# Kernel tuning notes

Hardware: AMD Instinct MI355X
Metric: run time of the kernel (lower is better)

## Reference

```python
import jax, jax.numpy as jnp
import numpy as np

N_NODES = 100000


def _gcn_conv(x, src, dst, ew, W, b, n_nodes):
    # PyG GCNConv: x' = D^{-1/2} (A + I) D^{-1/2} (x W) + b, with edge weights.
    h = x @ W  # [N, out]
    deg = jax.ops.segment_sum(ew, dst, num_segments=n_nodes)  # weighted in-degree
    dinv = jnp.where(deg > 0, jax.lax.rsqrt(deg), 0.0)
    norm = dinv[src] * ew * dinv[dst]  # [E]
    msg = h[src] * norm[:, None]  # gather + scale
    out = jax.ops.segment_sum(msg, dst, num_segments=n_nodes)  # scatter-add
    return out + b


def setup_inputs() -> dict:
    key = jax.random.key(0)
    ks = jax.random.split(key, 10)
    E = 1600000
    D_IN, H1, H2, D_OUT = 512, 128, 64, 1
    x = jax.random.normal(ks[0], (N_NODES, D_IN), dtype=jnp.float32)
    edge_index = jax.random.randint(ks[1], (2, E), 0, N_NODES, dtype=jnp.int64)
    edge_attr = jax.random.uniform(ks[2], (E,), dtype=jnp.float32)
    def glorot(k, fan_in, fan_out):
        s = jnp.sqrt(6.0 / (fan_in + fan_out))
        return jax.random.uniform(k, (fan_in, fan_out), minval=-s, maxval=s, dtype=jnp.float32)
    return {
        "x": x,
        "edge_index": edge_index,
        "edge_attr": edge_attr,
        "W1": glorot(ks[3], D_IN, H1), "b1": jnp.zeros((H1,), jnp.float32),
        "W2": glorot(ks[4], H1, H2), "b2": jnp.zeros((H2,), jnp.float32),
        "W3": glorot(ks[5], H2, D_OUT), "b3": jnp.zeros((D_OUT,), jnp.float32),
    }


def reference(x, edge_index, edge_attr, W1, b1, W2, b2, W3, b3):
    n = x.shape[0]
    # add self-loops with weight 1 (PyG GCNConv default)
    loops = jnp.arange(n, dtype=edge_index.dtype)
    src = jnp.concatenate([edge_index[0], loops])
    dst = jnp.concatenate([edge_index[1], loops])
    ew = jnp.concatenate([edge_attr, jnp.ones((n,), edge_attr.dtype)])
    h = _gcn_conv(x, src, dst, ew, W1, b1, n)
    h = jax.nn.relu(h)  # dropout is identity in eval mode
    h = _gcn_conv(h, src, dst, ew, W2, b2, n)
    h = jax.nn.relu(h)
    out = _gcn_conv(h, src, dst, ew, W3, b3, n)
    return out
```

## Files before the change

kernel.cpp:

```cpp
#include <hip/hip_runtime.h>

typedef __attribute__((ext_vector_type(4))) float f32x4;
typedef __attribute__((ext_vector_type(8))) short bf16x8;
typedef __attribute__((ext_vector_type(4))) unsigned short u16x4;

__device__ __forceinline__ unsigned short f2bf(float f) {
  unsigned int u = __builtin_bit_cast(unsigned int, f);
  u += 0x7fffu + ((u >> 16) & 1u);
  return (unsigned short)(u >> 16);
}
__device__ __forceinline__ float bf2f(unsigned short h) {
  unsigned int u = ((unsigned int)h) << 16;
  return __builtin_bit_cast(float, u);
}
__device__ __forceinline__ float bflo(unsigned int u) { return bf2f((unsigned short)(u & 0xffffu)); }
__device__ __forceinline__ float bfhi(unsigned int u) { return bf2f((unsigned short)(u >> 16)); }
__device__ __forceinline__ unsigned int packbf(float a, float b) {
  return (unsigned int)f2bf(a) | ((unsigned int)f2bf(b) << 16);
}

__global__ void hist_rank_k(const int* __restrict__ dst, int* __restrict__ cnt,
                            int* __restrict__ rank, int E) {
  int e = blockIdx.x * blockDim.x + threadIdx.x;
  if (e < E) rank[e] = atomicAdd(&cnt[dst[e]], 1);
}

__global__ void scan1_k(const int* __restrict__ cnt, int* __restrict__ row,
                        int* __restrict__ bsum, int N) {
  __shared__ int sh[256];
  const int tid = threadIdx.x;
  const int base = blockIdx.x * 2048 + tid * 8;
  int v[8]; int s = 0;
#pragma unroll
  for (int i = 0; i < 8; ++i) {
    int idx = base + i;
    v[i] = (idx < N) ? cnt[idx] : 0;
    s += v[i];
  }
  sh[tid] = s;
  __syncthreads();
  for (int off = 1; off < 256; off <<= 1) {
    int t = (tid >= off) ? sh[tid - off] : 0;
    __syncthreads();
    sh[tid] += t;
    __syncthreads();
  }
  int excl = sh[tid] - s;
  if (tid == 255) bsum[blockIdx.x] = sh[255];
  int run = excl;
#pragma unroll
  for (int i = 0; i < 8; ++i) {
    int idx = base + i;
    if (idx < N) row[idx] = run;
    run += v[i];
  }
}
__global__ void scan2_k(int* __restrict__ bsum, int nb) {
  if (threadIdx.x == 0 && blockIdx.x == 0) {
    int run = 0;
    for (int i = 0; i < nb; ++i) { int t = bsum[i]; bsum[i] = run; run += t; }
  }
}
__global__ void scan3_k(int* __restrict__ row, const int* __restrict__ bsum, int N, int E) {
  int idx = blockIdx.x * blockDim.x + threadIdx.x;
  if (idx < N) row[idx] += bsum[idx >> 11];
  if (idx == N) row[N] = E;
}
__global__ void scatter_nr_k(const int* __restrict__ src, const int* __restrict__ dst,
                             const float* __restrict__ ew, const int* __restrict__ row,
                             const int* __restrict__ rank, uint2* __restrict__ eadj, int E) {
  int e = blockIdx.x * blockDim.x + threadIdx.x;
  if (e >= E) return;
  int pos = row[dst[e]] + rank[e];
  eadj[pos] = make_uint2((unsigned)src[e], __builtin_bit_cast(unsigned, ew[e]));
}
__global__ void deg_dinv_k(const int* __restrict__ row, const uint2* __restrict__ eadj,
                           float* __restrict__ dinv, int N) {
  int n = blockIdx.x * blockDim.x + threadIdx.x;
  if (n >= N) return;
  float s = 1.0f;
  int end = row[n + 1];
  for (int e = row[n]; e < end; ++e) s += __builtin_bit_cast(float, eadj[e].y);
  dinv[n] = rsqrtf(s);
}
__global__ void fixnorm_k(const int* __restrict__ row, uint2* __restrict__ eadj,
                          const float* __restrict__ dinv, int N) {
  int n = blockIdx.x * blockDim.x + threadIdx.x;
  if (n >= N) return;
  float dd = dinv[n];
  int end = row[n + 1];
  for (int e = row[n]; e < end; ++e) {
    uint2 m = eadj[e];
    float nm = __builtin_bit_cast(float, m.y) * dinv[m.x] * dd;
    eadj[e].y = __builtin_bit_cast(unsigned, nm);
  }
}
__global__ void conv_wt2_k(const float* __restrict__ W1, unsigned short* __restrict__ Wt1,
                           const float* __restrict__ W2, unsigned short* __restrict__ Wt2) {
  int idx = blockIdx.x * blockDim.x + threadIdx.x;
  if (idx < 512 * 128) {
    int n = idx >> 9, k = idx & 511;
    Wt1[idx] = f2bf(W1[k * 128 + n]);
  } else {
    int j = idx - 512 * 128;
    if (j < 128 * 64) {
      int n = j >> 7, k = j & 127;
      Wt2[j] = f2bf(W2[k * 64 + n]);
    }
  }
}

template<int NC, int KD>
__launch_bounds__(256, 2)
__global__ void gemm_f32a_k(const float* __restrict__ A, const unsigned short* __restrict__ Wt,
                            unsigned short* __restrict__ Hb, int M) {
  constexpr int BM = 128, BK = 64;
  constexpr int WN = 64;
  constexpr int WGN = NC / WN;
  constexpr int WGM = 4 / WGN;
  constexpr int WM = BM / WGM;
  constexpr int FM = WM / 16;
  constexpr int FN = WN / 16;
  constexpr int KSUB = BK / 32;
  constexpr int A_PER_T = BM * (BK / 4) / 256;
  constexpr int B_PER_T = NC * (BK / 8) / 256;
  constexpr int nT = KD / BK;

  __shared__ unsigned short As[BM * BK];
  __shared__ unsigned short Bs[NC * BK];
  char* asb = reinterpret_cast<char*>(As);
  char* bsb = reinterpret_cast<char*>(Bs);

  const int tid = threadIdx.x;
  const int lane = tid & 63;
  const int wid = tid >> 6;
  const int wr = wid / WGN;
  const int wc = wid % WGN;
  const int lg = lane >> 4;
  const int lr = lane & 15;
  const int blockM = blockIdx.x * BM;

  float4 areg[A_PER_T];
  uint4 breg[B_PER_T];

  auto load_tiles = [&](int k0) {
#pragma unroll
    for (int i = 0; i < A_PER_T; ++i) {
      int chunk = tid + i * 256;
      int r = chunk >> 4, c4 = chunk & 15;
      int gr = blockM + r; if (gr >= M) gr = M - 1;
      areg[i] = *reinterpret_cast<const float4*>(A + (size_t)gr * KD + k0 + c4 * 4);
    }
#pragma unroll
    for (int i = 0; i < B_PER_T; ++i) {
      int chunk = tid + i * 256;
      int n = chunk >> 3, c = chunk & 7;
      breg[i] = *reinterpret_cast<const uint4*>(Wt + (size_t)n * KD + k0 + c * 8);
    }
  };

  f32x4 acc[FM][FN] = {};
  load_tiles(0);

  for (int t = 0; t < nT; ++t) {
    __syncthreads();
#pragma unroll
    for (int i = 0; i < A_PER_T; ++i) {
      int chunk = tid + i * 256;
      int r = chunk >> 4, c4 = chunk & 15;
      float4 v = areg[i];
      u16x4 p = { f2bf(v.x), f2bf(v.y), f2bf(v.z), f2bf(v.w) };
      int byte = r * (BK * 2) + ((c4 * 8) ^ ((r & 7) << 4));
      *reinterpret_cast<u16x4*>(asb + byte) = p;
    }
#pragma unroll
    for (int i = 0; i < B_PER_T; ++i) {
      int chunk = tid + i * 256;
      int n = chunk >> 3, c = chunk & 7;
      int byte = n * (BK * 2) + ((c * 16) ^ ((n & 7) << 4));
      *reinterpret_cast<uint4*>(bsb + byte) = breg[i];
    }
    __syncthreads();
    if (t + 1 < nT) load_tiles((t + 1) * BK);

    bf16x8 af[FM][KSUB], bfr[FN][KSUB];
#pragma unroll
    for (int fm = 0; fm < FM; ++fm)
#pragma unroll
      for (int kk = 0; kk < KSUB; ++kk) {
        int row = wr * WM + fm * 16 + lr;
        int k = kk * 32 + lg * 8;
        int byte = row * (BK * 2) + ((k * 2) ^ ((row & 7) << 4));
        af[fm][kk] = *reinterpret_cast<const bf16x8*>(asb + byte);
      }
#pragma unroll
    for (int fn = 0; fn < FN; ++fn)
#pragma unroll
      for (int kk = 0; kk < KSUB; ++kk) {
        int n = wc * WN + fn * 16 + lr;
        int k = kk * 32 + lg * 8;
        int byte = n * (BK * 2) + ((k * 2) ^ ((n & 7) << 4));
        bfr[fn][kk] = *reinterpret_cast<const bf16x8*>(bsb + byte);
      }
#pragma unroll
    for (int kk = 0; kk < KSUB; ++kk)
#pragma unroll
      for (int fm = 0; fm < FM; ++fm)
#pragma unroll
        for (int fn = 0; fn < FN; ++fn)
          acc[fm][fn] = __builtin_amdgcn_mfma_f32_16x16x32_bf16(
              af[fm][kk], bfr[fn][kk], acc[fm][fn], 0, 0, 0);
  }

#pragma unroll
  for (int fm = 0; fm < FM; ++fm)
#pragma unroll
    for (int fn = 0; fn < FN; ++fn) {
      int col = wc * WN + fn * 16 + lr;
#pragma unroll
      for (int j = 0; j < 4; ++j) {
        int row = blockM + wr * WM + fm * 16 + lg * 4 + j;
        if (row < M)
          Hb[(size_t)row * NC + col] = f2bf(acc[fm][fn][j]);
      }
    }
}

__launch_bounds__(256, 2)
__global__ void gemm_bf16a_k(const unsigned short* __restrict__ A,
                             const unsigned short* __restrict__ Wt,
                             unsigned short* __restrict__ Hb, int M) {
  constexpr int BM = 128, BK = 64, NC = 64, KD = 128;
  constexpr int WM = 32;
  constexpr int FM = 2, FN = 4, KSUB = 2;
  constexpr int A_PER_T = 4;
  constexpr int B_PER_T = 2;
  constexpr int nT = KD / BK;

  __shared__ unsigned short As[BM * BK];
  __shared__ unsigned short Bs[NC * BK];
  char* asb = reinterpret_cast<char*>(As);
  char* bsb = reinterpret_cast<char*>(Bs);

  const int tid = threadIdx.x;
  const int lane = tid & 63;
  const int wid = tid >> 6;
  const int lg = lane >> 4;
  const int lr = lane & 15;
  const int blockM = blockIdx.x * BM;

  uint4 areg[A_PER_T];
  uint4 breg[B_PER_T];

  auto load_tiles = [&](int k0) {
#pragma unroll
    for (int i = 0; i < A_PER_T; ++i) {
      int chunk = tid + i * 256;
      int r = chunk >> 3, c = chunk & 7;
      int gr = blockM + r; if (gr >= M) gr = M - 1;
      areg[i] = *reinterpret_cast<const uint4*>(A + (size_t)gr * KD + k0 + c * 8);
    }
#pragma unroll
    for (int i = 0; i < B_PER_T; ++i) {
      int chunk = tid + i * 256;
      int n = chunk >> 3, c = chunk & 7;
      breg[i] = *reinterpret_cast<const uint4*>(Wt + (size_t)n * KD + k0 + c * 8);
    }
  };

  f32x4 acc[FM][FN] = {};
  load_tiles(0);

  for (int t = 0; t < nT; ++t) {
    __syncthreads();
#pragma unroll
    for (int i = 0; i < A_PER_T; ++i) {
      int chunk = tid + i * 256;
      int r = chunk >> 3, c = chunk & 7;
      int byte = r * (BK * 2) + ((c * 16) ^ ((r & 7) << 4));
      *reinterpret_cast<uint4*>(asb + byte) = areg[i];
    }
#pragma unroll
    for (int i = 0; i < B_PER_T; ++i) {
      int chunk = tid + i * 256;
      int n = chunk >> 3, c = chunk & 7;
      int byte = n * (BK * 2) + ((c * 16) ^ ((n & 7) << 4));
      *reinterpret_cast<uint4*>(bsb + byte) = breg[i];
    }
    __syncthreads();
    if (t + 1 < nT) load_tiles((t + 1) * BK);

    bf16x8 af[FM][KSUB], bfr[FN][KSUB];
#pragma unroll
    for (int fm = 0; fm < FM; ++fm)
#pragma unroll
      for (int kk = 0; kk < KSUB; ++kk) {
        int row = wid * WM + fm * 16 + lr;
        int k = kk * 32 + lg * 8;
        int byte = row * (BK * 2) + ((k * 2) ^ ((row & 7) << 4));
        af[fm][kk] = *reinterpret_cast<const bf16x8*>(asb + byte);
      }
#pragma unroll
    for (int fn = 0; fn < FN; ++fn)
#pragma unroll
      for (int kk = 0; kk < KSUB; ++kk) {
        int n = fn * 16 + lr;
        int k = kk * 32 + lg * 8;
        int byte = n * (BK * 2) + ((k * 2) ^ ((n & 7) << 4));
        bfr[fn][kk] = *reinterpret_cast<const bf16x8*>(bsb + byte);
      }
#pragma unroll
    for (int kk = 0; kk < KSUB; ++kk)
#pragma unroll
      for (int fm = 0; fm < FM; ++fm)
#pragma unroll
        for (int fn = 0; fn < FN; ++fn)
          acc[fm][fn] = __builtin_amdgcn_mfma_f32_16x16x32_bf16(
              af[fm][kk], bfr[fn][kk], acc[fm][fn], 0, 0, 0);
  }

#pragma unroll
  for (int fm = 0; fm < FM; ++fm)
#pragma unroll
    for (int fn = 0; fn < FN; ++fn) {
      int col = fn * 16 + lr;
#pragma unroll
      for (int j = 0; j < 4; ++j) {
        int row = blockM + wid * WM + fm * 16 + lg * 4 + j;
        if (row < M)
          Hb[(size_t)row * NC + col] = f2bf(acc[fm][fn][j]);
      }
    }
}

__global__ void agg_csr128_k(const int* __restrict__ row, const uint2* __restrict__ eadj,
                             const unsigned short* __restrict__ h, const float* __restrict__ bias,
                             const float* __restrict__ dinv, unsigned int* __restrict__ o1b, int N) {
  const int lane = threadIdx.x & 63;
  const int node = blockIdx.x * (blockDim.x >> 6) + (threadIdx.x >> 6);
  if (node >= N) return;
  const unsigned int* hu = reinterpret_cast<const unsigned int*>(h);
  const int beg = row[node], end = row[node + 1];
  const float di = dinv[node];
  const float di2 = di * di;
  unsigned int hv = hu[(size_t)node * 64 + lane];
  float acc0 = bflo(hv) * di2;
  float acc1 = bfhi(hv) * di2;
  int e = beg;
  for (; e + 4 <= end; e += 4) {
    uint2 m0 = eadj[e], m1 = eadj[e + 1], m2 = eadj[e + 2], m3 = eadj[e + 3];
    int s0 = __builtin_amdgcn_readfirstlane(m0.x);
    int s1 = __builtin_amdgcn_readfirstlane(m1.x);
    int s2 = __builtin_amdgcn_readfirstlane(m2.x);
    int s3 = __builtin_amdgcn_readfirstlane(m3.x);
    float n0 = __builtin_bit_cast(float, __builtin_amdgcn_readfirstlane(m0.y));
    float n1 = __builtin_bit_cast(float, __builtin_amdgcn_readfirstlane(m1.y));
    float n2 = __builtin_bit_cast(float, __builtin_amdgcn_readfirstlane(m2.y));
    float n3 = __builtin_bit_cast(float, __builtin_amdgcn_readfirstlane(m3.y));
    unsigned int h0 = hu[(size_t)s0 * 64 + lane];
    unsigned int h1 = hu[(size_t)s1 * 64 + lane];
    unsigned int h2 = hu[(size_t)s2 * 64 + lane];
    unsigned int h3 = hu[(size_t)s3 * 64 + lane];
    acc0 += bflo(h0) * n0 + bflo(h1) * n1 + bflo(h2) * n2 + bflo(h3) * n3;
    acc1 += bfhi(h0) * n0 + bfhi(h1) * n1 + bfhi(h2) * n2 + bfhi(h3) * n3;
  }
  for (; e < end; ++e) {
    uint2 m0 = eadj[e];
    int s0 = __builtin_amdgcn_readfirstlane(m0.x);
    float n0 = __builtin_bit_cast(float, __builtin_amdgcn_readfirstlane(m0.y));
    unsigned int h0 = hu[(size_t)s0 * 64 + lane];
    acc0 += bflo(h0) * n0;
    acc1 += bfhi(h0) * n0;
  }
  float2 b = reinterpret_cast<const float2*>(bias)[lane];
  float r0 = fmaxf(acc0 + b.x, 0.f);
  float r1 = fmaxf(acc1 + b.y, 0.f);
  o1b[(size_t)node * 64 + lane] = packbf(r0, r1);
}

__global__ void agg_l23_k(const int* __restrict__ row, const uint2* __restrict__ eadj,
                          const unsigned short* __restrict__ h2, const float* __restrict__ b2,
                          const float* __restrict__ W3, const float* __restrict__ dinv,
                          float* __restrict__ h3, int N) {
  const int lane = threadIdx.x & 63;
  const int half = lane >> 5;
  const int l = lane & 31;
  const int node = blockIdx.x * (blockDim.x >> 6) + (threadIdx.x >> 6);
  if (node >= N) return;
  const unsigned int* hu = reinterpret_cast<const unsigned int*>(h2);
  const int beg = row[node], end = row[node + 1];
  float acc0 = 0.f, acc1 = 0.f;
  {
    const float di = dinv[node];
    unsigned int hv = hu[(size_t)node * 32 + l];
    float di2 = (half == 0) ? di * di : 0.f;
    acc0 = bflo(hv) * di2;
    acc1 = bfhi(hv) * di2;
  }
  int e = beg + half;
  for (; e + 2 < end; e += 4) {
    uint2 ma = eadj[e], mb = eadj[e + 2];
    float na = __builtin_bit_cast(float, ma.y);
    float nb = __builtin_bit_cast(float, mb.y);
    unsigned int ha = hu[(size_t)ma.x * 32 + l];
    unsigned int hb = hu[(size_t)mb.x * 32 + l];
    acc0 += bflo(ha) * na + bflo(hb) * nb;
    acc1 += bfhi(ha) * na + bfhi(hb) * nb;
  }
  if (e < end) {
    uint2 ma = eadj[e];
    float na = __builtin_bit_cast(float, ma.y);
    unsigned int ha = hu[(size_t)ma.x * 32 + l];
    acc0 += bflo(ha) * na;
    acc1 += bfhi(ha) * na;
  }
  acc0 += __shfl_xor(acc0, 32, 64);
  acc1 += __shfl_xor(acc1, 32, 64);
  float2 bb = reinterpret_cast<const float2*>(b2)[l];
  float2 w3 = reinterpret_cast<const float2*>(W3)[l];
  float v = fmaxf(acc0 + bb.x, 0.f) * w3.x + fmaxf(acc1 + bb.y, 0.f) * w3.y;
#pragma unroll
  for (int off = 16; off > 0; off >>= 1) v += __shfl_xor(v, off, 64);
  if (lane == 0) h3[node] = v;
}

__global__ void agg_csr1_k(const int* __restrict__ row, const uint2* __restrict__ eadj,
                           const float* __restrict__ h3, const float* __restrict__ b3,
                           const float* __restrict__ dinv, float* __restrict__ out, int N) {
  int n = blockIdx.x * blockDim.x + threadIdx.x;
  if (n >= N) return;
  float di = dinv[n];
  float acc = h3[n] * di * di;
  const int beg = row[n], end = row[n + 1];
  int e = beg;
  for (; e + 2 <= end; e += 2) {
    uint2 m0 = eadj[e], m1 = eadj[e + 1];
    acc += h3[m0.x] * __builtin_bit_cast(float, m0.y)
         + h3[m1.x] * __builtin_bit_cast(float, m1.y);
  }
  if (e < end) {
    uint2 m = eadj[e];
    acc += h3[m.x] * __builtin_bit_cast(float, m.y);
  }
  out[n] = acc + b3[0];
}

extern "C" void kernel_launch(void* const* d_in, const int* in_sizes, int n_in,
                              void* d_out, int out_size, void* d_ws, size_t ws_size,
                              hipStream_t stream) {
  const float* x  = (const float*)d_in[0];
  const int*   ei = (const int*)d_in[1];
  const float* ea = (const float*)d_in[2];
  const float* W1 = (const float*)d_in[3];
  const float* b1 = (const float*)d_in[4];
  const float* W2 = (const float*)d_in[5];
  const float* b2 = (const float*)d_in[6];
  const float* W3 = (const float*)d_in[7];
  const float* b3 = (const float*)d_in[8];
  float* out = (float*)d_out;

  const int N = in_sizes[0] / 512;
  const int E = in_sizes[2];
  const int* src = ei;
  const int* dst = ei + E;

  char* w = (char*)d_ws;
  auto alloc = [&](size_t bytes) {
    char* p = w; w += (bytes + 511) & ~(size_t)511; return p;
  };
  float* dinv         = (float*)alloc((size_t)N * 4);
  int*   cnt          = (int*)alloc((size_t)N * 4);
  int*   rowp         = (int*)alloc((size_t)(N + 1) * 4);
  int*   bsum         = (int*)alloc(4096 * 4);
  int*   rank         = (int*)alloc((size_t)E * 4);
  uint2* eadj         = (uint2*)alloc((size_t)E * 8);
  unsigned short* h1  = (unsigned short*)alloc((size_t)N * 128 * 2);
  unsigned int* o1b   = (unsigned int*)alloc((size_t)N * 64 * 4);
  unsigned short* h2  = (unsigned short*)alloc((size_t)N * 64 * 2);
  float* h3           = (float*)alloc((size_t)N * 4);
  unsigned short* wt1 = (unsigned short*)alloc(512 * 128 * 2);
  unsigned short* wt2 = (unsigned short*)alloc(128 * 64 * 2);

  const int TB = 256;
  const int nb_scan = (N + 2047) / 2048;

  hipMemsetAsync(cnt, 0, (size_t)N * 4, stream);

  hist_rank_k<<<(E + TB - 1) / TB, TB, 0, stream>>>(dst, cnt, rank, E);
  scan1_k<<<nb_scan, 256, 0, stream>>>(cnt, rowp, bsum, N);
  scan2_k<<<1, 64, 0, stream>>>(bsum, nb_scan);
  scan3_k<<<(N + 1 + TB - 1) / TB, TB, 0, stream>>>(rowp, bsum, N, E);
  scatter_nr_k<<<(E + TB - 1) / TB, TB, 0, stream>>>(src, dst, ea, rowp, rank, eadj, E);
  deg_dinv_k<<<(N + TB - 1) / TB, TB, 0, stream>>>(rowp, eadj, dinv, N);
  fixnorm_k<<<(N + TB - 1) / TB, TB, 0, stream>>>(rowp, eadj, dinv, N);
  conv_wt2_k<<<(512 * 128 + 128 * 64 + TB - 1) / TB, TB, 0, stream>>>(W1, wt1, W2, wt2);

  const int gblocks = (N + 127) / 128;
  const int ablocks = (N + 3) / 4;
  gemm_f32a_k<128, 512><<<gblocks, TB, 0, stream>>>(x, wt1, h1, N);
  agg_csr128_k<<<ablocks, TB, 0, stream>>>(rowp, eadj, h1, b1, dinv, o1b, N);
  gemm_bf16a_k<<<gblocks, TB, 0, stream>>>((const unsigned short*)o1b, wt2, h2, N);
  agg_l23_k<<<ablocks, TB, 0, stream>>>(rowp, eadj, h2, b2, W3, dinv, h3, N);
  agg_csr1_k<<<(N + TB - 1) / TB, TB, 0, stream>>>(rowp, eadj, h3, b3, dinv, out, N);
}
```

Baseline: 660.7 us.

## Fuse edge normalization into aggregation kernels and merge scan passes

Removes the fixnorm pass that rewrote per-edge normalized weights. Each aggregation kernel now computes ew*dinv[src]*dinv[dst] on the fly, with deeper unrolled batches of edge, dinv and feature loads. It also folds the serial block-sum scan into the offset-add kernel, where each block sums the preceding segment totals itself, saving a launch. The cost is an extra dinv gather per edge in all three aggregation layers, and readfirstlane scalarization is dropped in the 128-wide aggregation.

```diff
diff --git a/kernel.cpp b/kernel.cpp
--- a/kernel.cpp
+++ b/kernel.cpp
@@ -55,15 +55,17 @@
     run += v[i];
   }
 }
-__global__ void scan2_k(int* __restrict__ bsum, int nb) {
-  if (threadIdx.x == 0 && blockIdx.x == 0) {
-    int run = 0;
-    for (int i = 0; i < nb; ++i) { int t = bsum[i]; bsum[i] = run; run += t; }
-  }
-}
-__global__ void scan3_k(int* __restrict__ row, const int* __restrict__ bsum, int N, int E) {
+__global__ void scan23_k(int* __restrict__ row, const int* __restrict__ bsum, int N, int E) {
+  __shared__ int pref;
+  const int seg = (int)((blockIdx.x * blockDim.x) >> 11);
+  if (threadIdx.x == 0) {
+    int s = 0;
+    for (int i = 0; i < seg; ++i) s += bsum[i];
+    pref = s;
+  }
+  __syncthreads();
   int idx = blockIdx.x * blockDim.x + threadIdx.x;
-  if (idx < N) row[idx] += bsum[idx >> 11];
+  if (idx < N) row[idx] += pref;
   if (idx == N) row[N] = E;
 }
 __global__ void scatter_nr_k(const int* __restrict__ src, const int* __restrict__ dst,
@@ -82,18 +84,6 @@
   int end = row[n + 1];
   for (int e = row[n]; e < end; ++e) s += __builtin_bit_cast(float, eadj[e].y);
   dinv[n] = rsqrtf(s);
-}
-__global__ void fixnorm_k(const int* __restrict__ row, uint2* __restrict__ eadj,
-                          const float* __restrict__ dinv, int N) {
-  int n = blockIdx.x * blockDim.x + threadIdx.x;
-  if (n >= N) return;
-  float dd = dinv[n];
-  int end = row[n + 1];
-  for (int e = row[n]; e < end; ++e) {
-    uint2 m = eadj[e];
-    float nm = __builtin_bit_cast(float, m.y) * dinv[m.x] * dd;
-    eadj[e].y = __builtin_bit_cast(unsigned, nm);
-  }
 }
 __global__ void conv_wt2_k(const float* __restrict__ W1, unsigned short* __restrict__ Wt1,
                            const float* __restrict__ W2, unsigned short* __restrict__ Wt2) {
@@ -347,30 +337,27 @@
   float acc0 = bflo(hv) * di2;
   float acc1 = bfhi(hv) * di2;
   int e = beg;
-  for (; e + 4 <= end; e += 4) {
-    uint2 m0 = eadj[e], m1 = eadj[e + 1], m2 = eadj[e + 2], m3 = eadj[e + 3];
-    int s0 = __builtin_amdgcn_readfirstlane(m0.x);
-    int s1 = __builtin_amdgcn_readfirstlane(m1.x);
-    int s2 = __builtin_amdgcn_readfirstlane(m2.x);
-    int s3 = __builtin_amdgcn_readfirstlane(m3.x);
-    float n0 = __builtin_bit_cast(float, __builtin_amdgcn_readfirstlane(m0.y));
-    float n1 = __builtin_bit_cast(float, __builtin_amdgcn_readfirstlane(m1.y));
-    float n2 = __builtin_bit_cast(float, __builtin_amdgcn_readfirstlane(m2.y));
-    float n3 = __builtin_bit_cast(float, __builtin_amdgcn_readfirstlane(m3.y));
-    unsigned int h0 = hu[(size_t)s0 * 64 + lane];
-    unsigned int h1 = hu[(size_t)s1 * 64 + lane];
-    unsigned int h2 = hu[(size_t)s2 * 64 + lane];
-    unsigned int h3 = hu[(size_t)s3 * 64 + lane];
-    acc0 += bflo(h0) * n0 + bflo(h1) * n1 + bflo(h2) * n2 + bflo(h3) * n3;
-    acc1 += bfhi(h0) * n0 + bfhi(h1) * n1 + bfhi(h2) * n2 + bfhi(h3) * n3;
+  for (; e + 8 <= end; e += 8) {
+    uint2 m[8]; float dv[8]; unsigned int hh[8];
+#pragma unroll
+    for (int i = 0; i < 8; ++i) m[i] = eadj[e + i];
+#pragma unroll
+    for (int i = 0; i < 8; ++i) dv[i] = dinv[m[i].x];
+#pragma unroll
+    for (int i = 0; i < 8; ++i) hh[i] = hu[(size_t)m[i].x * 64 + lane];
+#pragma unroll
+    for (int i = 0; i < 8; ++i) {
+      float nm = __builtin_bit_cast(float, m[i].y) * dv[i] * di;
+      acc0 += bflo(hh[i]) * nm;
+      acc1 += bfhi(hh[i]) * nm;
+    }
   }
   for (; e < end; ++e) {
-    uint2 m0 = eadj[e];
-    int s0 = __builtin_amdgcn_readfirstlane(m0.x);
-    float n0 = __builtin_bit_cast(float, __builtin_amdgcn_readfirstlane(m0.y));
-    unsigned int h0 = hu[(size_t)s0 * 64 + lane];
-    acc0 += bflo(h0) * n0;
-    acc1 += bfhi(h0) * n0;
+    uint2 m = eadj[e];
+    float nm = __builtin_bit_cast(float, m.y) * dinv[m.x] * di;
+    unsigned int h0 = hu[(size_t)m.x * 64 + lane];
+    acc0 += bflo(h0) * nm;
+    acc1 += bfhi(h0) * nm;
   }
   float2 b = reinterpret_cast<const float2*>(bias)[lane];
   float r0 = fmaxf(acc0 + b.x, 0.f);
@@ -389,30 +376,36 @@
   if (node >= N) return;
   const unsigned int* hu = reinterpret_cast<const unsigned int*>(h2);
   const int beg = row[node], end = row[node + 1];
-  float acc0 = 0.f, acc1 = 0.f;
+  const float di = dinv[node];
+  float acc0, acc1;
   {
-    const float di = dinv[node];
     unsigned int hv = hu[(size_t)node * 32 + l];
     float di2 = (half == 0) ? di * di : 0.f;
     acc0 = bflo(hv) * di2;
     acc1 = bfhi(hv) * di2;
   }
   int e = beg + half;
-  for (; e + 2 < end; e += 4) {
-    uint2 ma = eadj[e], mb = eadj[e + 2];
-    float na = __builtin_bit_cast(float, ma.y);
-    float nb = __builtin_bit_cast(float, mb.y);
-    unsigned int ha = hu[(size_t)ma.x * 32 + l];
-    unsigned int hb = hu[(size_t)mb.x * 32 + l];
-    acc0 += bflo(ha) * na + bflo(hb) * nb;
-    acc1 += bfhi(ha) * na + bfhi(hb) * nb;
-  }
-  if (e < end) {
-    uint2 ma = eadj[e];
-    float na = __builtin_bit_cast(float, ma.y);
-    unsigned int ha = hu[(size_t)ma.x * 32 + l];
-    acc0 += bflo(ha) * na;
-    acc1 += bfhi(ha) * na;
+  for (; e + 6 < end; e += 8) {
+    uint2 m[4]; float dv[4]; unsigned int hh[4];
+#pragma unroll
+    for (int i = 0; i < 4; ++i) m[i] = eadj[e + 2 * i];
+#pragma unroll
+    for (int i = 0; i < 4; ++i) dv[i] = dinv[m[i].x];
+#pragma unroll
+    for (int i = 0; i < 4; ++i) hh[i] = hu[(size_t)m[i].x * 32 + l];
+#pragma unroll
+    for (int i = 0; i < 4; ++i) {
+      float nm = __builtin_bit_cast(float, m[i].y) * dv[i] * di;
+      acc0 += bflo(hh[i]) * nm;
+      acc1 += bfhi(hh[i]) * nm;
+    }
+  }
+  for (; e < end; e += 2) {
+    uint2 m = eadj[e];
+    float nm = __builtin_bit_cast(float, m.y) * dinv[m.x] * di;
+    unsigned int hv = hu[(size_t)m.x * 32 + l];
+    acc0 += bflo(hv) * nm;
+    acc1 += bfhi(hv) * nm;
   }
   acc0 += __shfl_xor(acc0, 32, 64);
   acc1 += __shfl_xor(acc1, 32, 64);
@@ -433,14 +426,22 @@
   float acc = h3[n] * di * di;
   const int beg = row[n], end = row[n + 1];
   int e = beg;
-  for (; e + 2 <= end; e += 2) {
-    uint2 m0 = eadj[e], m1 = eadj[e + 1];
-    acc += h3[m0.x] * __builtin_bit_cast(float, m0.y)
-         + h3[m1.x] * __builtin_bit_cast(float, m1.y);
-  }
-  if (e < end) {
+  for (; e + 4 <= end; e += 4) {
+    uint2 m[4]; float dv[4]; float hv[4];
+#pragma unroll
+    for (int i = 0; i < 4; ++i) m[i] = eadj[e + i];
+#pragma unroll
+    for (int i = 0; i < 4; ++i) dv[i] = dinv[m[i].x];
+#pragma unroll
+    for (int i = 0; i < 4; ++i) hv[i] = h3[m[i].x];
+#pragma unroll
+    for (int i = 0; i < 4; ++i)
+      acc += hv[i] * (__builtin_bit_cast(float, m[i].y) * dv[i] * di);
+  }
+  for (; e < end; ++e) {
     uint2 m = eadj[e];
-    acc += h3[m.x] * __builtin_bit_cast(float, m.y);
+    float nm = __builtin_bit_cast(float, m.y) * dinv[m.x] * di;
+    acc += h3[m.x] * nm;
   }
   out[n] = acc + b3[0];
 }
@@ -488,11 +489,9 @@
 
   hist_rank_k<<<(E + TB - 1) / TB, TB, 0, stream>>>(dst, cnt, rank, E);
   scan1_k<<<nb_scan, 256, 0, stream>>>(cnt, rowp, bsum, N);
-  scan2_k<<<1, 64, 0, stream>>>(bsum, nb_scan);
-  scan3_k<<<(N + 1 + TB - 1) / TB, TB, 0, stream>>>(rowp, bsum, N, E);
+  scan23_k<<<(N + 1 + TB - 1) / TB, TB, 0, stream>>>(rowp, bsum, N, E);
   scatter_nr_k<<<(E + TB - 1) / TB, TB, 0, stream>>>(src, dst, ea, rowp, rank, eadj, E);
   deg_dinv_k<<<(N + TB - 1) / TB, TB, 0, stream>>>(rowp, eadj, dinv, N);
-  fixnorm_k<<<(N + TB - 1) / TB, TB, 0, stream>>>(rowp, eadj, dinv, N);
   conv_wt2_k<<<(512 * 128 + 128 * 64 + TB - 1) / TB, TB, 0, stream>>>(W1, wt1, W2, wt2);
 
   const int gblocks = (N + 127) / 128;
```

Measured after the change: 640.0 us. -3.1%, faster.
